# Kernel optimization log

Measured on AMD Instinct MI355X. Metric: run time of the kernel, lower is better.

Reference implementation:

```python
import jax, jax.numpy as jnp
import numpy as np
import math

S = 8192
D = 128

def setup_inputs() -> dict:
    key = jax.random.key(0)
    kq, kk, kv = jax.random.split(key, 3)
    q = jax.random.normal(kq, (S, D), dtype=jnp.float32)
    k = jax.random.normal(kk, (S, D), dtype=jnp.float32)
    v = jax.random.normal(kv, (S, D), dtype=jnp.float32)
    return {"q": q, "k": k, "v": v}

def reference(q, k, v):
    # scores: [Sq, Sk], scaled by sqrt(head_dim)
    scale = 1.0 / math.sqrt(q.shape[1])
    scores = jnp.einsum('qd,kd->qk', q, k) * scale
    # causal mask: tril kept, strict upper triangle -> -inf (mask=True)
    causal = jnp.tril(jnp.ones((q.shape[0], k.shape[0]), dtype=bool))
    scores = jnp.where(causal, scores, -jnp.inf)
    # softmax over keys (dim=1), numerically stable
    attn = jax.nn.softmax(scores, axis=1)
    return jnp.einsum('qk,kd->qd', attn, v)
```

## Files before the change

### kernel.cpp

```cpp
#include <hip/hip_runtime.h>

#define S_TOTAL 8192
#define D_DIM   128
#define QBLK    128
#define KVBLK   64
#define QT64    64
#define TILEB   16384
#define QSCALE  0.12751879523178264f
#define NEG_BIG -1.0e30f
#define THR     8.0f

typedef __attribute__((ext_vector_type(8)))  short    bf16x8;
typedef __attribute__((ext_vector_type(16))) float    f32x16;
typedef __attribute__((ext_vector_type(4)))  unsigned u32x4;

static __device__ __forceinline__ unsigned short f2bf(float f) {
    unsigned int u = __builtin_bit_cast(unsigned int, f);
    u += 0x7FFFu + ((u >> 16) & 1u);
    return (unsigned short)(u >> 16);
}
static __device__ __forceinline__ float bf2f(unsigned short u) {
    return __builtin_bit_cast(float, (unsigned int)u << 16);
}
static __device__ __forceinline__ void glds16(const void* g, void* l) {
    __builtin_amdgcn_global_load_lds(
        (const __attribute__((address_space(1))) void*)g,
        (__attribute__((address_space(3))) void*)l, 16, 0, 0);
}
static __device__ __forceinline__ unsigned pk2(float lo, float hi) {
    unsigned r;
    asm("v_cvt_pk_bf16_f32 %0, %1, %2" : "=v"(r) : "v"(lo), "v"(hi));
    return r;
}
static __device__ __forceinline__ void pl32swap(unsigned& x, unsigned& y) {
    asm("v_permlane32_swap_b32 %0, %1" : "+v"(x), "+v"(y));
}

__global__ __launch_bounds__(256)
void prep_q(const float* __restrict__ Q, unsigned short* __restrict__ Qbf)
{
    int i4 = blockIdx.x * 256 + threadIdx.x;
    const float4 v = reinterpret_cast<const float4*>(Q)[i4];
    ushort4 o;
    o.x = f2bf(v.x * QSCALE); o.y = f2bf(v.y * QSCALE);
    o.z = f2bf(v.z * QSCALE); o.w = f2bf(v.w * QSCALE);
    reinterpret_cast<ushort4*>(Qbf)[i4] = o;
}

__global__ __launch_bounds__(256)
void prep_k(const float* __restrict__ K, unsigned short* __restrict__ Kswz)
{
    int c = blockIdx.x * 256 + threadIdx.x;
    int t = c >> 10;
    int r = (c >> 4) & 63;
    int slot = c & 15;
    int d0 = (slot ^ (r & 15)) << 3;
    const float* src = K + ((size_t)t * 64 + r) * D_DIM + d0;
    float4 a = *reinterpret_cast<const float4*>(src);
    float4 b = *reinterpret_cast<const float4*>(src + 4);
    bf16x8 o;
    o[0] = (short)f2bf(a.x); o[1] = (short)f2bf(a.y);
    o[2] = (short)f2bf(a.z); o[3] = (short)f2bf(a.w);
    o[4] = (short)f2bf(b.x); o[5] = (short)f2bf(b.y);
    o[6] = (short)f2bf(b.z); o[7] = (short)f2bf(b.w);
    *reinterpret_cast<bf16x8*>(&Kswz[(size_t)c * 8]) = o;
}

__global__ __launch_bounds__(256)
void prep_v(const float* __restrict__ V, unsigned short* __restrict__ Vt)
{
    __shared__ float sv[64 * 68];
    int t = blockIdx.x >> 1;
    int h = blockIdx.x & 1;
    #pragma unroll
    for (int it = 0; it < 4; ++it) {
        int f4 = it * 256 + threadIdx.x;
        int r   = f4 >> 4;
        int c16 = (f4 & 15) << 2;
        float4 v = *reinterpret_cast<const float4*>(
            V + ((size_t)t * 64 + r) * D_DIM + h * 64 + c16);
        sv[r * 68 + c16 + 0] = v.x;
        sv[r * 68 + c16 + 1] = v.y;
        sv[r * 68 + c16 + 2] = v.z;
        sv[r * 68 + c16 + 3] = v.w;
    }
    __syncthreads();
    #pragma unroll
    for (int ii = 0; ii < 2; ++ii) {
        int cl = threadIdx.x * 2 + ii;
        int dl = cl >> 3;
        int slot = cl & 7;
        int d = h * 64 + dl;
        int k0 = (slot ^ (d & 7)) << 3;
        bf16x8 o;
        #pragma unroll
        for (int i = 0; i < 8; ++i) o[i] = (short)f2bf(sv[(k0 + i) * 68 + dl]);
        *reinterpret_cast<bf16x8*>(&Vt[(size_t)t * 8192 + ((size_t)(d * 8 + slot)) * 8]) = o;
    }
}

__global__ __launch_bounds__(256, 2)
void attn32(const unsigned short* __restrict__ Qbf,
            const unsigned short* __restrict__ Kswz,
            const unsigned short* __restrict__ Vtswz,
            float* __restrict__ Og,
            unsigned short* __restrict__ Opart,
            float* __restrict__ mpart, float* __restrict__ lpart)
{
    __shared__ char sbuf[2][2 * TILEB];

    const int nsplit = (int)gridDim.x;
    const int split  = (int)blockIdx.x;
    const int qt     = (int)gridDim.y - 1 - (int)blockIdx.y;
    const int tid    = threadIdx.x;
    const int w      = tid >> 6;
    const int lane   = tid & 63;
    const int qc     = lane & 31;
    const int hi     = lane >> 5;

    const int qw_base = qt * QBLK + w * 32;
    const int qglob   = qw_base + qc;

    bf16x8 qf[8];
    #pragma unroll
    for (int dc = 0; dc < 8; ++dc)
        qf[dc] = *reinterpret_cast<const bf16x8*>(
            Qbf + (size_t)qglob * D_DIM + dc * 16 + hi * 8);

    f32x16 acc[4];
    #pragma unroll
    for (int dt = 0; dt < 4; ++dt)
        #pragma unroll
        for (int r = 0; r < 16; ++r) acc[dt][r] = 0.0f;
    float m_run = NEG_BIG, l_run = 0.0f;

    const int jtiles = 2 * qt + 2;

    auto STAGE = [&](int c, int j) {
        const char* gK = (const char*)Kswz + (size_t)j * TILEB;
        const char* gV = (const char*)Vtswz + (size_t)j * TILEB;
        char* lK = sbuf[c];
        char* lV = sbuf[c] + TILEB;
        #pragma unroll
        for (int it = 0; it < 4; ++it) {
            int goff = (it * 256 + tid) * 16;
            int loff = (it * 256 + (w << 6)) * 16;
            glds16(gK + goff, lK + loff);
            glds16(gV + goff, lV + loff);
        }
    };

    int j = split, c = 0;
    if (j < jtiles) {
        STAGE(0, j);
        __syncthreads();
        for (; j < jtiles; j += nsplit) {
            int jn = j + nsplit;
            if (jn < jtiles) STAGE(c ^ 1, jn);

            const char* bK = sbuf[c];
            const char* bV = sbuf[c] + TILEB;

            f32x16 sc[2];
            __builtin_amdgcn_s_setprio(1);
            #pragma unroll
            for (int kj = 0; kj < 2; ++kj) {
                f32x16 a;
                #pragma unroll
                for (int r = 0; r < 16; ++r) a[r] = 0.0f;
                int rK = kj * 32 + qc;
                #pragma unroll
                for (int dc = 0; dc < 8; ++dc) {
                    int slot = ((dc << 1) | hi) ^ (rK & 15);
                    bf16x8 kf = *reinterpret_cast<const bf16x8*>(
                        bK + (rK << 8) + (slot << 4));
                    a = __builtin_amdgcn_mfma_f32_32x32x16_bf16(kf, qf[dc], a, 0, 0, 0);
                }
                sc[kj] = a;
            }
            __builtin_amdgcn_s_setprio(0);

            if (j * 64 + 63 > qw_base) {
                #pragma unroll
                for (int kj = 0; kj < 2; ++kj)
                    #pragma unroll
                    for (int r = 0; r < 16; ++r) {
                        int kg = j * 64 + kj * 32 + (r & 3) + 8 * (r >> 2) + 4 * hi;
                        if (kg > qglob) sc[kj][r] = -INFINITY;
                    }
            }

            float mx = sc[0][0];
            #pragma unroll
            for (int r = 1; r < 16; ++r) mx = fmaxf(mx, sc[0][r]);
            #pragma unroll
            for (int r = 0; r < 16; ++r) mx = fmaxf(mx, sc[1][r]);
            float tmax = fmaxf(mx, __shfl_xor(mx, 32));

            if (__any(tmax > m_run + THR)) {
                float mnew = fmaxf(m_run, tmax);
                float fsc = __builtin_amdgcn_exp2f(m_run - mnew);
                m_run = mnew;
                l_run *= fsc;
                #pragma unroll
                for (int dt = 0; dt < 4; ++dt)
                    #pragma unroll
                    for (int r = 0; r < 16; ++r) acc[dt][r] *= fsc;
            }

            float lt = 0.0f;
            #pragma unroll
            for (int kj = 0; kj < 2; ++kj)
                #pragma unroll
                for (int r = 0; r < 16; ++r) {
                    float p = __builtin_amdgcn_exp2f(sc[kj][r] - m_run);
                    sc[kj][r] = p;
                    lt += p;
                }
            lt += __shfl_xor(lt, 32);
            l_run += lt;

            #pragma unroll
            for (int ck = 0; ck < 4; ++ck) {
                const int kjx = ck >> 1;
                const int rb  = (ck & 1) * 8;
                unsigned a = pk2(sc[kjx][rb + 0], sc[kjx][rb + 1]);
                unsigned b = pk2(sc[kjx][rb + 4], sc[kjx][rb + 5]);
                unsigned cc = pk2(sc[kjx][rb + 2], sc[kjx][rb + 3]);
                unsigned d = pk2(sc[kjx][rb + 6], sc[kjx][rb + 7]);
                pl32swap(a, b);
                pl32swap(cc, d);
                u32x4 t = {a, cc, b, d};
                bf16x8 pf = __builtin_bit_cast(bf16x8, t);

                __builtin_amdgcn_s_setprio(1);
                #pragma unroll
                for (int dt = 0; dt < 4; ++dt) {
                    int dV = dt * 32 + qc;
                    int slot = ((ck << 1) | hi) ^ (dV & 7);
                    bf16x8 vf = *reinterpret_cast<const bf16x8*>(
                        bV + (dV << 7) + (slot << 4));
                    acc[dt] = __builtin_amdgcn_mfma_f32_32x32x16_bf16(vf, pf, acc[dt], 0, 0, 0);
                }
                __builtin_amdgcn_s_setprio(0);
            }

            __syncthreads();
            c ^= 1;
        }
    }

    if (nsplit == 1) {
        float invl = 1.0f / l_run;
        #pragma unroll
        for (int dt = 0; dt < 4; ++dt)
            #pragma unroll
            for (int r = 0; r < 16; ++r) {
                int d = dt * 32 + (r & 3) + 8 * (r >> 2) + 4 * hi;
                Og[(size_t)qglob * D_DIM + d] = acc[dt][r] * invl;
            }
    } else {
        unsigned short* sO = reinterpret_cast<unsigned short*>(
            &sbuf[0][0]) + w * (32 * 136 + 16);
        #pragma unroll
        for (int dt = 0; dt < 4; ++dt)
            #pragma unroll
            for (int i = 0; i < 8; ++i) {
                unsigned pk = pk2(acc[dt][2 * i], acc[dt][2 * i + 1]);
                int d = dt * 32 + (i & 1) * 2 + (i >> 1) * 8 + 4 * hi;
                *reinterpret_cast<unsigned*>(&sO[qc * 136 + d]) = pk;
            }
        const int sidx = split;
        #pragma unroll
        for (int it = 0; it < 8; ++it) {
            int flat = it * 64 + lane;
            int q  = flat >> 4;
            int s8 = flat & 15;
            bf16x8 v = *reinterpret_cast<const bf16x8*>(&sO[q * 136 + s8 * 8]);
            *reinterpret_cast<bf16x8*>(
                Opart + ((size_t)sidx * S_TOTAL + qw_base + q) * D_DIM + s8 * 8) = v;
        }
        if (hi == 0) {
            mpart[(size_t)sidx * S_TOTAL + qglob] = m_run;
            lpart[(size_t)sidx * S_TOTAL + qglob] = l_run;
        }
    }
}

__global__ __launch_bounds__(256)
void attn_merge2(const unsigned short* __restrict__ Opart,
                 const float* __restrict__ mpart, const float* __restrict__ lpart,
                 float* __restrict__ Og, int nsplit)
{
    int tid = threadIdx.x;
    int row = blockIdx.x * 16 + (tid >> 4);
    int c8  = tid & 15;

    float M = NEG_BIG;
    for (int s = 0; s < nsplit; ++s)
        M = fmaxf(M, mpart[(size_t)s * S_TOTAL + row]);
    float L = 0.0f;
    for (int s = 0; s < nsplit; ++s)
        L += __builtin_amdgcn_exp2f(mpart[(size_t)s * S_TOTAL + row] - M)
             * lpart[(size_t)s * S_TOTAL + row];
    float invL = 1.0f / L;

    float a[8] = {0.f, 0.f, 0.f, 0.f, 0.f, 0.f, 0.f, 0.f};
    for (int s = 0; s < nsplit; ++s) {
        float e = __builtin_amdgcn_exp2f(mpart[(size_t)s * S_TOTAL + row] - M);
        bf16x8 o = *reinterpret_cast<const bf16x8*>(
            &Opart[((size_t)s * S_TOTAL + row) * D_DIM + c8 * 8]);
        #pragma unroll
        for (int i = 0; i < 8; ++i)
            a[i] += e * bf2f((unsigned short)o[i]);
    }
    float4 w0 = {a[0] * invL, a[1] * invL, a[2] * invL, a[3] * invL};
    float4 w1 = {a[4] * invL, a[5] * invL, a[6] * invL, a[7] * invL};
    float* dst = Og + (size_t)row * D_DIM + c8 * 8;
    *reinterpret_cast<float4*>(dst)     = w0;
    *reinterpret_cast<float4*>(dst + 4) = w1;
}

typedef __attribute__((ext_vector_type(4))) float f32x4;

__global__ __launch_bounds__(256, 2)
void attn_f32(const float* __restrict__ Qg, const float* __restrict__ Kg,
              const float* __restrict__ Vg, float* __restrict__ Og)
{
    __shared__ unsigned short sK [64 * 128];
    __shared__ unsigned short sVt[128 * 64];
    __shared__ unsigned short sP [4 * 16 * 72];

    const int qt   = (int)gridDim.y - 1 - (int)blockIdx.y;
    const int tid  = threadIdx.x;
    const int w    = tid >> 6;
    const int lane = tid & 63;
    const int g    = lane >> 4;
    const int lr   = lane & 15;

    const int qrow_base  = qt * 64 + w * 16 + g * 4;
    const int q_frag_row = qt * 64 + w * 16 + lr;

    bf16x8 qa[4];
    #pragma unroll
    for (int dc = 0; dc < 4; ++dc) {
        const float* src = Qg + q_frag_row * D_DIM + dc * 32 + g * 8;
        bf16x8 v;
        #pragma unroll
        for (int i = 0; i < 8; ++i) v[i] = (short)f2bf(src[i]);
        qa[dc] = v;
    }

    f32x4 acc[8];
    #pragma unroll
    for (int dj = 0; dj < 8; ++dj) acc[dj] = f32x4{0.f, 0.f, 0.f, 0.f};
    float m_run[4], l_run[4];
    #pragma unroll
    for (int r = 0; r < 4; ++r) { m_run[r] = -INFINITY; l_run[r] = 0.0f; }

    const float scale = 0.08838834764831845f;
    const int jtiles = qt + 1;
    unsigned short* sPw = sP + w * (16 * 72);
    char* sKc = reinterpret_cast<char*>(sK);
    char* sVc = reinterpret_cast<char*>(sVt);

    for (int j = 0; j < jtiles; ++j) {
        __syncthreads();
        #pragma unroll
        for (int it = 0; it < 8; ++it) {
            int flat4 = it * 256 + tid;
            int r  = flat4 >> 5;
            int d0 = (flat4 & 31) << 2;
            const float4 kv = *reinterpret_cast<const float4*>(
                Kg + (j * 64 + r) * D_DIM + d0);
            ushort4 wv;
            wv.x = f2bf(kv.x); wv.y = f2bf(kv.y); wv.z = f2bf(kv.z); wv.w = f2bf(kv.w);
            int byte = (r << 8) | (((d0 >> 3) ^ (r & 15)) << 4) | ((d0 & 7) << 1);
            *reinterpret_cast<ushort4*>(sKc + byte) = wv;
        }
        {
            int d = tid & 127;
            int khalf = tid >> 7;
            #pragma unroll
            for (int it = 0; it < 8; ++it) {
                int k0 = it * 8 + khalf * 4;
                const float* vsrc = Vg + (j * 64 + k0) * D_DIM + d;
                ushort4 wv;
                wv.x = f2bf(vsrc[0 * D_DIM]); wv.y = f2bf(vsrc[1 * D_DIM]);
                wv.z = f2bf(vsrc[2 * D_DIM]); wv.w = f2bf(vsrc[3 * D_DIM]);
                int byte = (d << 7) | (((k0 >> 3) ^ (d & 7)) << 4) | ((k0 & 7) << 1);
                *reinterpret_cast<ushort4*>(sVc + byte) = wv;
            }
        }
        __syncthreads();

        f32x4 sf[4];
        #pragma unroll
        for (int kj = 0; kj < 4; ++kj) {
            f32x4 accs = f32x4{0.f, 0.f, 0.f, 0.f};
            #pragma unroll
            for (int dc = 0; dc < 4; ++dc) {
                int rowk = kj * 16 + lr;
                int slot = (dc * 4 + g) ^ lr;
                bf16x8 b = *reinterpret_cast<bf16x8*>(sKc + ((rowk << 8) | (slot << 4)));
                accs = __builtin_amdgcn_mfma_f32_16x16x32_bf16(qa[dc], b, accs, 0, 0, 0);
            }
            sf[kj] = accs;
        }
        #pragma unroll
        for (int kj = 0; kj < 4; ++kj)
            #pragma unroll
            for (int r = 0; r < 4; ++r)
                sf[kj][r] *= scale;
        if (j == qt) {
            #pragma unroll
            for (int kj = 0; kj < 4; ++kj) {
                int kglob = j * 64 + kj * 16 + lr;
                #pragma unroll
                for (int r = 0; r < 4; ++r)
                    if (kglob > qrow_base + r) sf[kj][r] = -INFINITY;
            }
        }
        float tmax[4];
        #pragma unroll
        for (int r = 0; r < 4; ++r)
            tmax[r] = fmaxf(fmaxf(sf[0][r], sf[1][r]), fmaxf(sf[2][r], sf[3][r]));
        #pragma unroll
        for (int off = 1; off < 16; off <<= 1)
            #pragma unroll
            for (int r = 0; r < 4; ++r)
                tmax[r] = fmaxf(tmax[r], __shfl_xor(tmax[r], off));
        float fsc[4], lt[4];
        #pragma unroll
        for (int r = 0; r < 4; ++r) {
            float mn = fmaxf(m_run[r], tmax[r]);
            fsc[r] = __expf(m_run[r] - mn);
            m_run[r] = mn;
            lt[r] = 0.0f;
        }
        #pragma unroll
        for (int kj = 0; kj < 4; ++kj)
            #pragma unroll
            for (int r = 0; r < 4; ++r) {
                float p = __expf(sf[kj][r] - m_run[r]);
                sf[kj][r] = p;
                lt[r] += p;
            }
        #pragma unroll
        for (int off = 1; off < 16; off <<= 1)
            #pragma unroll
            for (int r = 0; r < 4; ++r)
                lt[r] += __shfl_xor(lt[r], off);
        #pragma unroll
        for (int r = 0; r < 4; ++r)
            l_run[r] = l_run[r] * fsc[r] + lt[r];
        #pragma unroll
        for (int dj = 0; dj < 8; ++dj)
            #pragma unroll
            for (int r = 0; r < 4; ++r)
                acc[dj][r] *= fsc[r];
        #pragma unroll
        for (int kj = 0; kj < 4; ++kj)
            #pragma unroll
            for (int r = 0; r < 4; ++r)
                sPw[(g * 4 + r) * 72 + kj * 16 + lr] = f2bf(sf[kj][r]);
        bf16x8 pa[2];
        #pragma unroll
        for (int kc = 0; kc < 2; ++kc)
            pa[kc] = *reinterpret_cast<bf16x8*>(sPw + lr * 72 + kc * 32 + g * 8);
        #pragma unroll
        for (int dj = 0; dj < 8; ++dj) {
            #pragma unroll
            for (int kc = 0; kc < 2; ++kc) {
                int d = dj * 16 + lr;
                int slot = (kc * 4 + g) ^ (lr & 7);
                bf16x8 b = *reinterpret_cast<bf16x8*>(sVc + ((d << 7) | (slot << 4)));
                acc[dj] = __builtin_amdgcn_mfma_f32_16x16x32_bf16(pa[kc], b, acc[dj], 0, 0, 0);
            }
        }
    }
    #pragma unroll
    for (int r = 0; r < 4; ++r) {
        float inv = 1.0f / l_run[r];
        int row = qrow_base + r;
        #pragma unroll
        for (int dj = 0; dj < 8; ++dj)
            Og[row * D_DIM + dj * 16 + lr] = acc[dj][r] * inv;
    }
}

extern "C" void kernel_launch(void* const* d_in, const int* in_sizes, int n_in,
                              void* d_out, int out_size, void* d_ws, size_t ws_size,
                              hipStream_t stream)
{
    const float* Qg = (const float*)d_in[0];
    const float* Kg = (const float*)d_in[1];
    const float* Vg = (const float*)d_in[2];
    float* Og = (float*)d_out;

    const size_t bfElems = (size_t)S_TOTAL * D_DIM;
    auto need = [bfElems](int n) -> size_t {
        size_t base = 3 * bfElems * 2;
        if (n > 1)
            base += (size_t)n * (bfElems * 2 + (size_t)S_TOTAL * 8);
        return base;
    };

    if (d_ws == nullptr || ws_size < need(1)) {
        hipLaunchKernelGGL(attn_f32, dim3(1, 128), dim3(256), 0, stream,
                           Qg, Kg, Vg, Og);
        return;
    }

    int nsplit = 16;
    while (nsplit > 1 && ws_size < need(nsplit)) nsplit >>= 1;

    unsigned short* Qbf  = (unsigned short*)d_ws;
    unsigned short* Kswz = Qbf + bfElems;
    unsigned short* Vt   = Kswz + bfElems;
    unsigned short* Opart = Vt + bfElems;
    float* mpart = (float*)(Opart + (size_t)nsplit * bfElems);
    float* lpart = mpart + (size_t)nsplit * S_TOTAL;

    hipLaunchKernelGGL(prep_q, dim3(1024), dim3(256), 0, stream, Qg, Qbf);
    hipLaunchKernelGGL(prep_k, dim3(512),  dim3(256), 0, stream, Kg, Kswz);
    hipLaunchKernelGGL(prep_v, dim3(256),  dim3(256), 0, stream, Vg, Vt);

    hipLaunchKernelGGL(attn32, dim3(nsplit, QT64), dim3(256), 0, stream,
                       Qbf, Kswz, Vt, Og, Opart, mpart, lpart);
    if (nsplit > 1)
        hipLaunchKernelGGL(attn_merge2, dim3(S_TOTAL / 16), dim3(256), 0, stream,
                           Opart, mpart, lpart, Og, nsplit);
}
```

Before: 60.11 us.

## Use 256-row Q tiles with 8 waves and causal-balanced variable split-KV

```diff
diff --git a/kernel.cpp b/kernel.cpp
--- a/kernel.cpp
+++ b/kernel.cpp
@@ -2,16 +2,18 @@
 
 #define S_TOTAL 8192
 #define D_DIM   128
-#define QBLK    128
+#define QBLK    256
+#define NQT     32
 #define KVBLK   64
-#define QT64    64
 #define TILEB   16384
+#define NUNITS  435
 #define QSCALE  0.12751879523178264f
 #define NEG_BIG -1.0e30f
 #define THR     8.0f
 
 typedef __attribute__((ext_vector_type(8)))  short    bf16x8;
 typedef __attribute__((ext_vector_type(16))) float    f32x16;
+typedef __attribute__((ext_vector_type(4)))  float    f32x4;
 typedef __attribute__((ext_vector_type(4)))  unsigned u32x4;
 
 static __device__ __forceinline__ unsigned short f2bf(float f) {
@@ -35,6 +37,7 @@
 static __device__ __forceinline__ void pl32swap(unsigned& x, unsigned& y) {
     asm("v_permlane32_swap_b32 %0, %1" : "+v"(x), "+v"(y));
 }
+static __device__ __forceinline__ int spl_of(int qt) { return (4 * qt + 8) / 5; }
 
 __global__ __launch_bounds__(256)
 void prep_q(const float* __restrict__ Q, unsigned short* __restrict__ Qbf)
@@ -99,24 +102,31 @@
     }
 }
 
-__global__ __launch_bounds__(256, 2)
-void attn32(const unsigned short* __restrict__ Qbf,
-            const unsigned short* __restrict__ Kswz,
-            const unsigned short* __restrict__ Vtswz,
-            float* __restrict__ Og,
-            unsigned short* __restrict__ Opart,
-            float* __restrict__ mpart, float* __restrict__ lpart)
+__global__ __launch_bounds__(512, 4)
+void attn8(const unsigned short* __restrict__ Qbf,
+           const unsigned short* __restrict__ Kswz,
+           const unsigned short* __restrict__ Vtswz,
+           unsigned short* __restrict__ Opart,
+           float* __restrict__ mpart, float* __restrict__ lpart)
 {
     __shared__ char sbuf[2][2 * TILEB];
 
-    const int nsplit = (int)gridDim.x;
-    const int split  = (int)blockIdx.x;
-    const int qt     = (int)gridDim.y - 1 - (int)blockIdx.y;
-    const int tid    = threadIdx.x;
-    const int w      = tid >> 6;
-    const int lane   = tid & 63;
-    const int qc     = lane & 31;
-    const int hi     = lane >> 5;
+    int b = (int)blockIdx.x, qt = 0, split = 0;
+    for (int t = NQT - 1; t >= 0; --t) {
+        int s = spl_of(t);
+        if (b < s) { qt = t; split = b; break; }
+        b -= s;
+    }
+    const int SPLITS = spl_of(qt);
+    int ubase = 0;
+    for (int i = 0; i < qt; ++i) ubase += spl_of(i);
+    const int unit = ubase + split;
+
+    const int tid  = threadIdx.x;
+    const int w    = tid >> 6;
+    const int lane = tid & 63;
+    const int qc   = lane & 31;
+    const int hi   = lane >> 5;
 
     const int qw_base = qt * QBLK + w * 32;
     const int qglob   = qw_base + qc;
@@ -134,7 +144,7 @@
         for (int r = 0; r < 16; ++r) acc[dt][r] = 0.0f;
     float m_run = NEG_BIG, l_run = 0.0f;
 
-    const int jtiles = 2 * qt + 2;
+    const int jtiles = 4 * qt + 4;
 
     auto STAGE = [&](int c, int j) {
         const char* gK = (const char*)Kswz + (size_t)j * TILEB;
@@ -142,174 +152,172 @@
         char* lK = sbuf[c];
         char* lV = sbuf[c] + TILEB;
         #pragma unroll
-        for (int it = 0; it < 4; ++it) {
-            int goff = (it * 256 + tid) * 16;
-            int loff = (it * 256 + (w << 6)) * 16;
+        for (int it = 0; it < 2; ++it) {
+            int goff = (it * 512 + tid) * 16;
+            int loff = (it * 512 + (w << 6)) * 16;
             glds16(gK + goff, lK + loff);
             glds16(gV + goff, lV + loff);
         }
     };
 
     int j = split, c = 0;
-    if (j < jtiles) {
-        STAGE(0, j);
-        __syncthreads();
-        for (; j < jtiles; j += nsplit) {
-            int jn = j + nsplit;
-            if (jn < jtiles) STAGE(c ^ 1, jn);
-
-            const char* bK = sbuf[c];
-            const char* bV = sbuf[c] + TILEB;
-
-            f32x16 sc[2];
-            __builtin_amdgcn_s_setprio(1);
-            #pragma unroll
-            for (int kj = 0; kj < 2; ++kj) {
-                f32x16 a;
+    STAGE(0, j);
+    __syncthreads();
+    for (; j < jtiles; j += SPLITS) {
+        int jn = j + SPLITS;
+        if (jn < jtiles) STAGE(c ^ 1, jn);
+
+        const char* bK = sbuf[c];
+        const char* bV = sbuf[c] + TILEB;
+
+        #pragma unroll
+        for (int kj = 0; kj < 2; ++kj) {
+            const int kbase = j * 64 + kj * 32;
+            if (kbase <= qw_base + 31) {
+                f32x16 sc;
                 #pragma unroll
-                for (int r = 0; r < 16; ++r) a[r] = 0.0f;
-                int rK = kj * 32 + qc;
+                for (int r = 0; r < 16; ++r) sc[r] = 0.0f;
+                const int rK = kj * 32 + qc;
+                __builtin_amdgcn_s_setprio(1);
                 #pragma unroll
                 for (int dc = 0; dc < 8; ++dc) {
                     int slot = ((dc << 1) | hi) ^ (rK & 15);
                     bf16x8 kf = *reinterpret_cast<const bf16x8*>(
                         bK + (rK << 8) + (slot << 4));
-                    a = __builtin_amdgcn_mfma_f32_32x32x16_bf16(kf, qf[dc], a, 0, 0, 0);
+                    sc = __builtin_amdgcn_mfma_f32_32x32x16_bf16(kf, qf[dc], sc, 0, 0, 0);
                 }
-                sc[kj] = a;
-            }
-            __builtin_amdgcn_s_setprio(0);
-
-            if (j * 64 + 63 > qw_base) {
-                #pragma unroll
-                for (int kj = 0; kj < 2; ++kj)
+                __builtin_amdgcn_s_setprio(0);
+
+                if (kbase + 31 > qw_base) {
                     #pragma unroll
                     for (int r = 0; r < 16; ++r) {
-                        int kg = j * 64 + kj * 32 + (r & 3) + 8 * (r >> 2) + 4 * hi;
-                        if (kg > qglob) sc[kj][r] = -INFINITY;
+                        int kg = kbase + (r & 3) + 8 * (r >> 2) + 4 * hi;
+                        if (kg > qglob) sc[r] = -INFINITY;
                     }
-            }
-
-            float mx = sc[0][0];
-            #pragma unroll
-            for (int r = 1; r < 16; ++r) mx = fmaxf(mx, sc[0][r]);
-            #pragma unroll
-            for (int r = 0; r < 16; ++r) mx = fmaxf(mx, sc[1][r]);
-            float tmax = fmaxf(mx, __shfl_xor(mx, 32));
-
-            if (__any(tmax > m_run + THR)) {
-                float mnew = fmaxf(m_run, tmax);
-                float fsc = __builtin_amdgcn_exp2f(m_run - mnew);
-                m_run = mnew;
-                l_run *= fsc;
+                }
+
+                float m0 = fmaxf(fmaxf(sc[0],  sc[1]),  fmaxf(sc[2],  sc[3]));
+                float m1 = fmaxf(fmaxf(sc[4],  sc[5]),  fmaxf(sc[6],  sc[7]));
+                float m2 = fmaxf(fmaxf(sc[8],  sc[9]),  fmaxf(sc[10], sc[11]));
+                float m3 = fmaxf(fmaxf(sc[12], sc[13]), fmaxf(sc[14], sc[15]));
+                float mx = fmaxf(fmaxf(m0, m1), fmaxf(m2, m3));
+                float tmax = fmaxf(mx, __shfl_xor(mx, 32));
+
+                if (__any(tmax > m_run + THR)) {
+                    float mnew = fmaxf(m_run, tmax);
+                    float fs = __builtin_amdgcn_exp2f(m_run - mnew);
+                    m_run = mnew;
+                    l_run *= fs;
+                    #pragma unroll
+                    for (int dt = 0; dt < 4; ++dt)
+                        #pragma unroll
+                        for (int r = 0; r < 16; ++r) acc[dt][r] *= fs;
+                }
+
+                float s0 = 0.f, s1 = 0.f, s2 = 0.f, s3 = 0.f;
                 #pragma unroll
-                for (int dt = 0; dt < 4; ++dt)
+                for (int r = 0; r < 16; r += 4) {
+                    float p0 = __builtin_amdgcn_exp2f(sc[r + 0] - m_run);
+                    float p1 = __builtin_amdgcn_exp2f(sc[r + 1] - m_run);
+                    float p2 = __builtin_amdgcn_exp2f(sc[r + 2] - m_run);
+                    float p3 = __builtin_amdgcn_exp2f(sc[r + 3] - m_run);
+                    sc[r + 0] = p0; sc[r + 1] = p1; sc[r + 2] = p2; sc[r + 3] = p3;
+                    s0 += p0; s1 += p1; s2 += p2; s3 += p3;
+                }
+                float lt = (s0 + s1) + (s2 + s3);
+                lt += __shfl_xor(lt, 32);
+                l_run += lt;
+
+                #pragma unroll
+                for (int cl = 0; cl < 2; ++cl) {
+                    const int rb = cl * 8;
+                    const int ck = kj * 2 + cl;
+                    unsigned a  = pk2(sc[rb + 0], sc[rb + 1]);
+                    unsigned bb = pk2(sc[rb + 4], sc[rb + 5]);
+                    unsigned cc = pk2(sc[rb + 2], sc[rb + 3]);
+                    unsigned d  = pk2(sc[rb + 6], sc[rb + 7]);
+                    pl32swap(a, bb);
+                    pl32swap(cc, d);
+                    u32x4 t4 = {a, cc, bb, d};
+                    bf16x8 pf = __builtin_bit_cast(bf16x8, t4);
+
+                    __builtin_amdgcn_s_setprio(1);
                     #pragma unroll
-                    for (int r = 0; r < 16; ++r) acc[dt][r] *= fsc;
-            }
-
-            float lt = 0.0f;
-            #pragma unroll
-            for (int kj = 0; kj < 2; ++kj)
+                    for (int dt = 0; dt < 4; ++dt) {
+                        int dV = dt * 32 + qc;
+                        int slot = ((ck << 1) | hi) ^ (dV & 7);
+                        bf16x8 vf = *reinterpret_cast<const bf16x8*>(
+                            bV + (dV << 7) + (slot << 4));
+                        acc[dt] = __builtin_amdgcn_mfma_f32_32x32x16_bf16(vf, pf, acc[dt], 0, 0, 0);
+                    }
+                    __builtin_amdgcn_s_setprio(0);
+                }
+            }
+        }
+        __syncthreads();
+        c ^= 1;
+    }
+
+    unsigned short* OB = Opart + (size_t)unit * (QBLK * D_DIM);
+    #pragma unroll
+    for (int ph = 0; ph < 2; ++ph) {
+        __syncthreads();
+        if ((w >> 2) == ph) {
+            unsigned short* sO = reinterpret_cast<unsigned short*>(&sbuf[0][0])
+                                 + (w & 3) * (32 * 136 + 16);
+            #pragma unroll
+            for (int dt = 0; dt < 4; ++dt)
                 #pragma unroll
-                for (int r = 0; r < 16; ++r) {
-                    float p = __builtin_amdgcn_exp2f(sc[kj][r] - m_run);
-                    sc[kj][r] = p;
-                    lt += p;
+                for (int i = 0; i < 8; ++i) {
+                    unsigned pk = pk2(acc[dt][2 * i], acc[dt][2 * i + 1]);
+                    int d = dt * 32 + (i & 1) * 2 + (i >> 1) * 8 + 4 * hi;
+                    *reinterpret_cast<unsigned*>(&sO[qc * 136 + d]) = pk;
                 }
-            lt += __shfl_xor(lt, 32);
-            l_run += lt;
-
-            #pragma unroll
-            for (int ck = 0; ck < 4; ++ck) {
-                const int kjx = ck >> 1;
-                const int rb  = (ck & 1) * 8;
-                unsigned a = pk2(sc[kjx][rb + 0], sc[kjx][rb + 1]);
-                unsigned b = pk2(sc[kjx][rb + 4], sc[kjx][rb + 5]);
-                unsigned cc = pk2(sc[kjx][rb + 2], sc[kjx][rb + 3]);
-                unsigned d = pk2(sc[kjx][rb + 6], sc[kjx][rb + 7]);
-                pl32swap(a, b);
-                pl32swap(cc, d);
-                u32x4 t = {a, cc, b, d};
-                bf16x8 pf = __builtin_bit_cast(bf16x8, t);
-
-                __builtin_amdgcn_s_setprio(1);
-                #pragma unroll
-                for (int dt = 0; dt < 4; ++dt) {
-                    int dV = dt * 32 + qc;
-                    int slot = ((ck << 1) | hi) ^ (dV & 7);
-                    bf16x8 vf = *reinterpret_cast<const bf16x8*>(
-                        bV + (dV << 7) + (slot << 4));
-                    acc[dt] = __builtin_amdgcn_mfma_f32_32x32x16_bf16(vf, pf, acc[dt], 0, 0, 0);
-                }
-                __builtin_amdgcn_s_setprio(0);
-            }
-
-            __syncthreads();
-            c ^= 1;
-        }
-    }
-
-    if (nsplit == 1) {
-        float invl = 1.0f / l_run;
-        #pragma unroll
-        for (int dt = 0; dt < 4; ++dt)
-            #pragma unroll
-            for (int r = 0; r < 16; ++r) {
-                int d = dt * 32 + (r & 3) + 8 * (r >> 2) + 4 * hi;
-                Og[(size_t)qglob * D_DIM + d] = acc[dt][r] * invl;
-            }
-    } else {
-        unsigned short* sO = reinterpret_cast<unsigned short*>(
-            &sbuf[0][0]) + w * (32 * 136 + 16);
-        #pragma unroll
-        for (int dt = 0; dt < 4; ++dt)
-            #pragma unroll
-            for (int i = 0; i < 8; ++i) {
-                unsigned pk = pk2(acc[dt][2 * i], acc[dt][2 * i + 1]);
-                int d = dt * 32 + (i & 1) * 2 + (i >> 1) * 8 + 4 * hi;
-                *reinterpret_cast<unsigned*>(&sO[qc * 136 + d]) = pk;
-            }
-        const int sidx = split;
-        #pragma unroll
-        for (int it = 0; it < 8; ++it) {
-            int flat = it * 64 + lane;
-            int q  = flat >> 4;
-            int s8 = flat & 15;
-            bf16x8 v = *reinterpret_cast<const bf16x8*>(&sO[q * 136 + s8 * 8]);
-            *reinterpret_cast<bf16x8*>(
-                Opart + ((size_t)sidx * S_TOTAL + qw_base + q) * D_DIM + s8 * 8) = v;
-        }
-        if (hi == 0) {
-            mpart[(size_t)sidx * S_TOTAL + qglob] = m_run;
-            lpart[(size_t)sidx * S_TOTAL + qglob] = l_run;
-        }
+            #pragma unroll
+            for (int it = 0; it < 8; ++it) {
+                int flat = it * 64 + lane;
+                int q  = flat >> 4;
+                int s8 = flat & 15;
+                bf16x8 v = *reinterpret_cast<const bf16x8*>(&sO[q * 136 + s8 * 8]);
+                *reinterpret_cast<bf16x8*>(
+                    OB + ((size_t)(w * 32 + q)) * D_DIM + s8 * 8) = v;
+            }
+        }
+    }
+    if (hi == 0) {
+        mpart[unit * QBLK + w * 32 + qc] = m_run;
+        lpart[unit * QBLK + w * 32 + qc] = l_run;
     }
 }
 
 __global__ __launch_bounds__(256)
-void attn_merge2(const unsigned short* __restrict__ Opart,
+void attn_mergeV(const unsigned short* __restrict__ Opart,
                  const float* __restrict__ mpart, const float* __restrict__ lpart,
-                 float* __restrict__ Og, int nsplit)
+                 float* __restrict__ Og)
 {
     int tid = threadIdx.x;
     int row = blockIdx.x * 16 + (tid >> 4);
     int c8  = tid & 15;
+    int qt    = row >> 8;
+    int local = row & 255;
+    int splits = spl_of(qt);
+    int ubase = 0;
+    for (int i = 0; i < qt; ++i) ubase += spl_of(i);
 
     float M = NEG_BIG;
-    for (int s = 0; s < nsplit; ++s)
-        M = fmaxf(M, mpart[(size_t)s * S_TOTAL + row]);
+    for (int s = 0; s < splits; ++s)
+        M = fmaxf(M, mpart[(size_t)(ubase + s) * QBLK + local]);
     float L = 0.0f;
-    for (int s = 0; s < nsplit; ++s)
-        L += __builtin_amdgcn_exp2f(mpart[(size_t)s * S_TOTAL + row] - M)
-             * lpart[(size_t)s * S_TOTAL + row];
+    for (int s = 0; s < splits; ++s)
+        L += __builtin_amdgcn_exp2f(mpart[(size_t)(ubase + s) * QBLK + local] - M)
+             * lpart[(size_t)(ubase + s) * QBLK + local];
     float invL = 1.0f / L;
 
     float a[8] = {0.f, 0.f, 0.f, 0.f, 0.f, 0.f, 0.f, 0.f};
-    for (int s = 0; s < nsplit; ++s) {
-        float e = __builtin_amdgcn_exp2f(mpart[(size_t)s * S_TOTAL + row] - M);
+    for (int s = 0; s < splits; ++s) {
+        float e = __builtin_amdgcn_exp2f(mpart[(size_t)(ubase + s) * QBLK + local] - M);
         bf16x8 o = *reinterpret_cast<const bf16x8*>(
-            &Opart[((size_t)s * S_TOTAL + row) * D_DIM + c8 * 8]);
+            &Opart[((size_t)(ubase + s) * QBLK + local) * D_DIM + c8 * 8]);
         #pragma unroll
         for (int i = 0; i < 8; ++i)
             a[i] += e * bf2f((unsigned short)o[i]);
@@ -320,8 +328,6 @@
     *reinterpret_cast<float4*>(dst)     = w0;
     *reinterpret_cast<float4*>(dst + 4) = w1;
 }
-
-typedef __attribute__((ext_vector_type(4))) float f32x4;
 
 __global__ __launch_bounds__(256, 2)
 void attn_f32(const float* __restrict__ Qg, const float* __restrict__ Kg,
@@ -499,36 +505,29 @@
     float* Og = (float*)d_out;
 
     const size_t bfElems = (size_t)S_TOTAL * D_DIM;
-    auto need = [bfElems](int n) -> size_t {
-        size_t base = 3 * bfElems * 2;
-        if (n > 1)
-            base += (size_t)n * (bfElems * 2 + (size_t)S_TOTAL * 8);
-        return base;
-    };
-
-    if (d_ws == nullptr || ws_size < need(1)) {
+    const size_t need = 3 * bfElems * 2
+                      + (size_t)NUNITS * ((size_t)QBLK * D_DIM * 2
+                                          + (size_t)QBLK * 8);
+
+    if (d_ws == nullptr || ws_size < need) {
         hipLaunchKernelGGL(attn_f32, dim3(1, 128), dim3(256), 0, stream,
                            Qg, Kg, Vg, Og);
         return;
     }
 
-    int nsplit = 16;
-    while (nsplit > 1 && ws_size < need(nsplit)) nsplit >>= 1;
-
-    unsigned short* Qbf  = (unsigned short*)d_ws;
-    unsigned short* Kswz = Qbf + bfElems;
-    unsigned short* Vt   = Kswz + bfElems;
+    unsigned short* Qbf   = (unsigned short*)d_ws;
+    unsigned short* Kswz  = Qbf + bfElems;
+    unsigned short* Vt    = Kswz + bfElems;
     unsigned short* Opart = Vt + bfElems;
-    float* mpart = (float*)(Opart + (size_t)nsplit * bfElems);
-    float* lpart = mpart + (size_t)nsplit * S_TOTAL;
+    float* mpart = (float*)(Opart + (size_t)NUNITS * QBLK * D_DIM);
+    float* lpart = mpart + (size_t)NUNITS * QBLK;
 
     hipLaunchKernelGGL(prep_q, dim3(1024), dim3(256), 0, stream, Qg, Qbf);
     hipLaunchKernelGGL(prep_k, dim3(512),  dim3(256), 0, stream, Kg, Kswz);
     hipLaunchKernelGGL(prep_v, dim3(256),  dim3(256), 0, stream, Vg, Vt);
 
-    hipLaunchKernelGGL(attn32, dim3(nsplit, QT64), dim3(256), 0, stream,
-                       Qbf, Kswz, Vt, Og, Opart, mpart, lpart);
-    if (nsplit > 1)
-        hipLaunchKernelGGL(attn_merge2, dim3(S_TOTAL / 16), dim3(256), 0, stream,
-                           Opart, mpart, lpart, Og, nsplit);
-}
+    hipLaunchKernelGGL(attn8, dim3(NUNITS), dim3(512), 0, stream,
+                       Qbf, Kswz, Vt, Opart, mpart, lpart);
+    hipLaunchKernelGGL(attn_mergeV, dim3(S_TOTAL / 16), dim3(256), 0, stream,
+                       Opart, mpart, lpart, Og);
+}
```

Result: slower. 92.76 us (+54.3%).
